# Optimization experiments

Hardware: AMD Instinct MI355X
Metric: run time of the kernel (lower is better)

## Reference

```python
import jax, jax.numpy as jnp
import numpy as np

B, C, T, S, E = 8, 1024, 2048, 2048, 1024
SCALE = 0.7071067811865476  # sqrt(0.5), as in ConvS2S


def setup_inputs() -> dict:
    key = jax.random.key(0)
    ks = jax.random.split(key, 8)
    return {
        "conved": jax.random.normal(ks[0], (B, C, T), jnp.float32),
        "encoder_conved": jax.random.normal(ks[1], (B, S, E), jnp.float32),
        "encoder_combined": jax.random.normal(ks[2], (B, S, E), jnp.float32),
        "x": jax.random.normal(ks[3], (B, T, E), jnp.float32),
        "scale": jnp.float32(SCALE),
        # attn_hid2emb: Linear(out_channels -> emb_dim); torch weight is [out, in]
        "W_h2e": jax.random.normal(ks[4], (E, C), jnp.float32) * 0.02,
        "b_h2e": jnp.zeros((E,), jnp.float32),
        # attn_emb2hid: Linear(emb_dim -> out_channels)
        "W_e2h": jax.random.normal(ks[5], (C, E), jnp.float32) * 0.02,
        "b_e2h": jnp.zeros((C,), jnp.float32),
    }


def reference(conved, encoder_conved, encoder_combined, x, scale,
              W_h2e, b_h2e, W_e2h, b_e2h):
    # conved: [B, C, T] -> project to embedding space: [B, T, E]
    conved_emb = jnp.einsum('bct,ec->bte', conved, W_h2e) + b_h2e
    conved_combined = (conved_emb + x) * scale            # [B, T, E]
    # energy = Q @ K^T : [B, T, S]
    energy = jnp.einsum('bte,bse->bts', conved_combined, encoder_conved)
    attention = jax.nn.softmax(energy, axis=-1)           # [B, T, S]
    # attended encoding = A @ V : [B, T, E]
    attended = jnp.einsum('bts,bse->bte', attention, encoder_combined)
    # project back to hidden: [B, T, C]
    attended = jnp.einsum('bte,ce->btc', attended, W_e2h) + b_e2h
    # residual in channels-first layout: [B, C, T]
    attended_combined = conved + attended.transpose(0, 2, 1)
    return attention, attended_combined
```

## Files before the change

### kernel.cpp

```cpp
#include <hip/hip_runtime.h>
#include <hip/hip_bf16.h>

typedef unsigned short u16;
typedef __attribute__((ext_vector_type(8))) short bf16x8;
typedef __attribute__((ext_vector_type(4))) float f32x4;

#define B_ 8
#define C_ 1024
#define T_ 2048
#define S_ 2048
#define E_ 1024

__device__ __forceinline__ u16 f2bf(float v) {
    __hip_bfloat16 h = __float2bfloat16(v);
    return *reinterpret_cast<u16*>(&h);
}
__device__ __forceinline__ float bf2f(u16 u) {
    __hip_bfloat16 h = *reinterpret_cast<__hip_bfloat16*>(&u);
    return __bfloat162float(h);
}
__device__ __forceinline__ void split2(float v, u16& h, u16& l) {
    h = f2bf(v);
    l = f2bf(v - bf2f(h));
}

__device__ __forceinline__ void async16(const u16* g, u16* l) {
    __builtin_amdgcn_global_load_lds((const __attribute__((address_space(1))) void*)g,
                                     (__attribute__((address_space(3))) void*)l, 16, 0, 0);
}

template<int EPI, bool SPLIT3>
__global__ __launch_bounds__(256, 2) void gemm_bt(
    const u16* __restrict__ Ahi, const u16* __restrict__ Alo,
    const u16* __restrict__ Bhi, const u16* __restrict__ Blo,
    int Kdim, long sA, long sB, int N,
    float* __restrict__ outF, long sOutF,
    u16* __restrict__ outB, u16* __restrict__ outB2, long sOutB,
    const float* __restrict__ bias,
    const float* __restrict__ add, long sAdd,
    const float* __restrict__ scale_ptr)
{
    __shared__ u16 smem[(SPLIT3 ? 4 : 2) * 4096];
    u16* As_hi = smem;
    u16* Bs_hi = smem + 4096;
    u16* As_lo = SPLIT3 ? (smem + 8192)  : smem;
    u16* Bs_lo = SPLIT3 ? (smem + 12288) : smem;

    const int b  = blockIdx.z;
    const int bm = blockIdx.y * 128;
    const int bn = blockIdx.x * 128;
    const u16* Ah = Ahi + (size_t)b * sA;
    const u16* Bh = Bhi + (size_t)b * sB;
    const u16* Al = SPLIT3 ? (Alo + (size_t)b * sA) : nullptr;
    const u16* Bl = SPLIT3 ? (Blo + (size_t)b * sB) : nullptr;

    const int tid  = threadIdx.x;
    const int w    = tid >> 6, lane = tid & 63;
    const int wr   = w >> 1,   wc   = w & 1;
    const int lr   = lane & 15, ls  = lane >> 4;

    const int srow  = lane >> 2;
    const int sslot = lane & 3;
    const int kk    = ((sslot ^ ((srow >> 1) & 3)) << 3);
    const size_t gA0 = (size_t)(bm + w * 16 + srow) * Kdim + kk;
    const size_t gA1 = (size_t)(bm + (w + 4) * 16 + srow) * Kdim + kk;
    const size_t gB0 = (size_t)(bn + w * 16 + srow) * Kdim + kk;
    const size_t gB1 = (size_t)(bn + (w + 4) * 16 + srow) * Kdim + kk;
    const int l0 = w * 512, l1 = (w + 4) * 512;

    f32x4 acc[4][4];
    #pragma unroll
    for (int m = 0; m < 4; m++) {
        #pragma unroll
        for (int n = 0; n < 4; n++) {
            f32x4 z = {0.f, 0.f, 0.f, 0.f};
            acc[m][n] = z;
        }
    }

    const int foff = ((ls ^ ((lr >> 1) & 3)) << 3);

    for (int k0 = 0; k0 < Kdim; k0 += 32) {
        async16(Ah + gA0 + k0, As_hi + l0);
        async16(Ah + gA1 + k0, As_hi + l1);
        async16(Bh + gB0 + k0, Bs_hi + l0);
        async16(Bh + gB1 + k0, Bs_hi + l1);
        if constexpr (SPLIT3) {
            async16(Al + gA0 + k0, As_lo + l0);
            async16(Al + gA1 + k0, As_lo + l1);
            async16(Bl + gB0 + k0, Bs_lo + l0);
            async16(Bl + gB1 + k0, Bs_lo + l1);
        }
        asm volatile("s_waitcnt vmcnt(0)" ::: "memory");
        __syncthreads();

        bf16x8 ah[4], al[4];
        #pragma unroll
        for (int m = 0; m < 4; m++) {
            int off = (wr * 64 + m * 16 + lr) * 32 + foff;
            ah[m] = *(const bf16x8*)(As_hi + off);
            if constexpr (SPLIT3) al[m] = *(const bf16x8*)(As_lo + off);
        }
        #pragma unroll
        for (int n = 0; n < 4; n++) {
            int off = (wc * 64 + n * 16 + lr) * 32 + foff;
            bf16x8 bh = *(const bf16x8*)(Bs_hi + off);
            if constexpr (SPLIT3) {
                bf16x8 bl = *(const bf16x8*)(Bs_lo + off);
                #pragma unroll
                for (int m = 0; m < 4; m++)
                    acc[m][n] = __builtin_amdgcn_mfma_f32_16x16x32_bf16(ah[m], bh, acc[m][n], 0, 0, 0);
                #pragma unroll
                for (int m = 0; m < 4; m++)
                    acc[m][n] = __builtin_amdgcn_mfma_f32_16x16x32_bf16(ah[m], bl, acc[m][n], 0, 0, 0);
                #pragma unroll
                for (int m = 0; m < 4; m++)
                    acc[m][n] = __builtin_amdgcn_mfma_f32_16x16x32_bf16(al[m], bh, acc[m][n], 0, 0, 0);
            } else {
                #pragma unroll
                for (int m = 0; m < 4; m++)
                    acc[m][n] = __builtin_amdgcn_mfma_f32_16x16x32_bf16(ah[m], bh, acc[m][n], 0, 0, 0);
            }
        }
        __syncthreads();
    }

    float scl = 1.0f;
    if constexpr (EPI == 0) scl = *scale_ptr;

    #pragma unroll
    for (int m = 0; m < 4; m++) {
        #pragma unroll
        for (int n = 0; n < 4; n++) {
            const int Rb = bm + wr * 64 + m * 16 + ls * 4;
            const int Cc = bn + wc * 64 + n * 16 + lr;
            f32x4 v = acc[m][n];
            #pragma unroll
            for (int j = 0; j < 4; j++) {
                const int R = Rb + j;
                const size_t o = (size_t)R * N + Cc;
                float val = v[j];
                if constexpr (EPI == 0) {
                    val = (val + bias[Cc] + add[(size_t)b * sAdd + o]) * scl;
                    u16 h, l;
                    split2(val, h, l);
                    outB[(size_t)b * sOutB + o]  = h;
                    outB2[(size_t)b * sOutB + o] = l;
                } else if constexpr (EPI == 1) {
                    outF[(size_t)b * sOutF + o] = val;
                } else if constexpr (EPI == 2) {
                    outB[(size_t)b * sOutB + o] = f2bf(val);
                } else {
                    outF[(size_t)b * sOutF + o] = val + bias[R] + add[(size_t)b * sAdd + o];
                }
            }
        }
    }
}


template<bool SPLIT>
__global__ __launch_bounds__(256) void split_cast_kernel(
    const float* __restrict__ in, u16* __restrict__ hi, u16* __restrict__ lo, long n4)
{
    long i = (long)blockIdx.x * blockDim.x + threadIdx.x;
    long stride = (long)gridDim.x * blockDim.x;
    const float4* in4 = (const float4*)in;
    ushort4* h4 = (ushort4*)hi;
    ushort4* l4 = (ushort4*)lo;
    for (; i < n4; i += stride) {
        float4 v = in4[i];
        ushort4 h, l;
        split2(v.x, h.x, l.x);
        split2(v.y, h.y, l.y);
        split2(v.z, h.z, l.z);
        split2(v.w, h.w, l.w);
        h4[i] = h;
        if constexpr (SPLIT) l4[i] = l;
    }
}

template<bool SPLIT>
__global__ __launch_bounds__(256) void transpose_split_kernel(
    const float* __restrict__ in, u16* __restrict__ hi, u16* __restrict__ lo, int R, int Cc)
{
    __shared__ float tile[32][33];
    const size_t boff = (size_t)blockIdx.z * R * Cc;
    const int c0 = blockIdx.x * 32;
    const int r0 = blockIdx.y * 32;
    const int tx = threadIdx.x, ty = threadIdx.y;
    #pragma unroll
    for (int i = ty; i < 32; i += 8)
        tile[i][tx] = in[boff + (size_t)(r0 + i) * Cc + c0 + tx];
    __syncthreads();
    #pragma unroll
    for (int i = ty; i < 32; i += 8) {
        float v = tile[tx][i];
        size_t o = boff + (size_t)(c0 + i) * R + r0 + tx;
        u16 h, l;
        split2(v, h, l);
        hi[o] = h;
        if constexpr (SPLIT) lo[o] = l;
    }
}

__device__ __forceinline__ float wred_max(float v) {
    #pragma unroll
    for (int off = 32; off; off >>= 1) v = fmaxf(v, __shfl_xor(v, off, 64));
    return v;
}
__device__ __forceinline__ float wred_sum(float v) {
    #pragma unroll
    for (int off = 32; off; off >>= 1) v += __shfl_xor(v, off, 64);
    return v;
}

__global__ __launch_bounds__(256) void softmax_kernel(float* __restrict__ att, u16* __restrict__ attB)
{
    __shared__ float red[4];
    const size_t row = blockIdx.x;
    float* p  = att  + row * (size_t)S_;
    u16*   pb = attB + row * (size_t)S_;
    const int t = threadIdx.x, w = t >> 6, lane = t & 63;

    float4 v0 = ((const float4*)p)[t];
    float4 v1 = ((const float4*)p)[t + 256];
    float m = fmaxf(fmaxf(fmaxf(v0.x, v0.y), fmaxf(v0.z, v0.w)),
                    fmaxf(fmaxf(v1.x, v1.y), fmaxf(v1.z, v1.w)));
    m = wred_max(m);
    if (lane == 0) red[w] = m;
    __syncthreads();
    m = fmaxf(fmaxf(red[0], red[1]), fmaxf(red[2], red[3]));
    __syncthreads();

    float e0 = __expf(v0.x - m), e1 = __expf(v0.y - m), e2 = __expf(v0.z - m), e3 = __expf(v0.w - m);
    float e4 = __expf(v1.x - m), e5 = __expf(v1.y - m), e6 = __expf(v1.z - m), e7 = __expf(v1.w - m);
    float s = ((e0 + e1) + (e2 + e3)) + ((e4 + e5) + (e6 + e7));
    s = wred_sum(s);
    if (lane == 0) red[w] = s;
    __syncthreads();
    s = (red[0] + red[1]) + (red[2] + red[3]);
    const float inv = 1.0f / s;

    float4 o0 = {e0 * inv, e1 * inv, e2 * inv, e3 * inv};
    float4 o1 = {e4 * inv, e5 * inv, e6 * inv, e7 * inv};
    ((float4*)p)[t]       = o0;
    ((float4*)p)[t + 256] = o1;
    ushort4 b0, b1;
    b0.x = f2bf(o0.x); b0.y = f2bf(o0.y); b0.z = f2bf(o0.z); b0.w = f2bf(o0.w);
    b1.x = f2bf(o1.x); b1.y = f2bf(o1.y); b1.z = f2bf(o1.z); b1.w = f2bf(o1.w);
    ((ushort4*)pb)[t]       = b0;
    ((ushort4*)pb)[t + 256] = b1;
}

extern "C" void kernel_launch(void* const* d_in, const int* in_sizes, int n_in,
                              void* d_out, int out_size, void* d_ws, size_t ws_size,
                              hipStream_t stream)
{
    (void)in_sizes; (void)n_in; (void)out_size; (void)ws_size;
    const float* conved = (const float*)d_in[0];
    const float* encK   = (const float*)d_in[1];
    const float* encV   = (const float*)d_in[2];
    const float* x      = (const float*)d_in[3];
    const float* scale  = (const float*)d_in[4];
    const float* W_h2e  = (const float*)d_in[5];
    const float* b_h2e  = (const float*)d_in[6];
    const float* W_e2h  = (const float*)d_in[7];
    const float* b_e2h  = (const float*)d_in[8];

    float* attn = (float*)d_out;
    float* out2 = attn + (size_t)B_ * T_ * S_;

    const size_t NBT = (size_t)B_ * T_ * E_;
    char* p = (char*)d_ws;
    auto take = [&](size_t bytes) { char* r = p; p += bytes; return (u16*)r; };

    u16* Qhi  = take(NBT * 2);
    u16* Qlo  = take(NBT * 2);
    u16* Khi  = take(NBT * 2);
    u16* Klo  = take(NBT * 2);
    u16* Vt   = take(NBT * 2);
    u16* Whi  = take((size_t)E_ * C_ * 2);
    u16* Wlo  = take((size_t)E_ * C_ * 2);
    u16* We2h = take((size_t)C_ * E_ * 2);
    u16* CThi = take(NBT * 2);
    u16* CTlo = take(NBT * 2);
    u16* attnB = CThi;
    u16* Aemb  = Qhi;

    dim3 blk256(256);
    dim3 tblk(32, 8);

    transpose_split_kernel<true ><<<dim3(T_ / 32, C_ / 32, B_), tblk, 0, stream>>>(conved, CThi, CTlo, C_, T_);
    split_cast_kernel<true >     <<<dim3(512),  blk256, 0, stream>>>(W_h2e, Whi, Wlo, (long)E_ * C_ / 4);
    split_cast_kernel<true >     <<<dim3(2048), blk256, 0, stream>>>(encK, Khi, Klo, (long)B_ * S_ * E_ / 4);
    transpose_split_kernel<false><<<dim3(E_ / 32, S_ / 32, B_), tblk, 0, stream>>>(encV, Vt, nullptr, S_, E_);
    split_cast_kernel<false>     <<<dim3(512),  blk256, 0, stream>>>(W_e2h, We2h, nullptr, (long)C_ * E_ / 4);

    gemm_bt<0, true><<<dim3(E_ / 128, T_ / 128, B_), blk256, 0, stream>>>(
        CThi, CTlo, Whi, Wlo, C_, (long)T_ * C_, 0L, E_,
        nullptr, 0L, Qhi, Qlo, (long)T_ * E_, b_h2e, x, (long)T_ * E_, scale);

    gemm_bt<1, true><<<dim3(S_ / 128, T_ / 128, B_), blk256, 0, stream>>>(
        Qhi, Qlo, Khi, Klo, E_, (long)T_ * E_, (long)S_ * E_, S_,
        attn, (long)T_ * S_, nullptr, nullptr, 0L, nullptr, nullptr, 0L, nullptr);

    softmax_kernel<<<dim3(B_ * T_), blk256, 0, stream>>>(attn, attnB);

    gemm_bt<2, false><<<dim3(E_ / 128, T_ / 128, B_), blk256, 0, stream>>>(
        attnB, nullptr, Vt, nullptr, S_, (long)T_ * S_, (long)E_ * S_, E_,
        nullptr, 0L, Aemb, nullptr, (long)T_ * E_, nullptr, nullptr, 0L, nullptr);

    gemm_bt<3, false><<<dim3(T_ / 128, C_ / 128, B_), blk256, 0, stream>>>(
        We2h, nullptr, Aemb, nullptr, E_, 0L, (long)T_ * E_, T_,
        out2, (long)C_ * T_, nullptr, nullptr, 0L, b_e2h, conved, (long)C_ * T_, nullptr);
}
```

Baseline: 935.7 us.

## Remap GEMM tiles across XCDs, raise occupancy hint, vectorize transpose kernel

The GEMM kernel now remaps its flattened block index so that consecutive tiles land on the same XCD, which should improve L2 reuse of A and B rows across the chiplets. Its launch bounds hint also rises from 2 to 4 workgroups per CU, which may force register spilling. The transpose/split kernel switches to float4 loads and ushort4 stores with an 8x32 thread block. The tile reads after the transpose now hit the same LDS bank for lanes with different tx (stride 4*33), which can cause bank conflicts.

```diff
diff --git a/kernel.cpp b/kernel.cpp
--- a/kernel.cpp
+++ b/kernel.cpp
@@ -30,7 +30,7 @@
 }
 
 template<int EPI, bool SPLIT3>
-__global__ __launch_bounds__(256, 2) void gemm_bt(
+__global__ __launch_bounds__(256, 4) void gemm_bt(
     const u16* __restrict__ Ahi, const u16* __restrict__ Alo,
     const u16* __restrict__ Bhi, const u16* __restrict__ Blo,
     int Kdim, long sA, long sB, int N,
@@ -46,9 +46,18 @@
     u16* As_lo = SPLIT3 ? (smem + 8192)  : smem;
     u16* Bs_lo = SPLIT3 ? (smem + 12288) : smem;
 
+    const int gx = gridDim.x;
+    const int nwg = gx * gridDim.y;
+    int f = blockIdx.y * gx + blockIdx.x;
+    {
+        const int q = nwg >> 3, r = nwg & 7;
+        const int xcd = f & 7, idx = f >> 3;
+        f = (xcd < r ? xcd * (q + 1) : r * (q + 1) + (xcd - r) * q) + idx;
+    }
     const int b  = blockIdx.z;
-    const int bm = blockIdx.y * 128;
-    const int bn = blockIdx.x * 128;
+    const int bm = (f / gx) * 128;
+    const int bn = (f % gx) * 128;
+
     const u16* Ah = Ahi + (size_t)b * sA;
     const u16* Bh = Bhi + (size_t)b * sB;
     const u16* Al = SPLIT3 ? (Alo + (size_t)b * sA) : nullptr;
@@ -188,20 +197,24 @@
     const size_t boff = (size_t)blockIdx.z * R * Cc;
     const int c0 = blockIdx.x * 32;
     const int r0 = blockIdx.y * 32;
-    const int tx = threadIdx.x, ty = threadIdx.y;
-    #pragma unroll
-    for (int i = ty; i < 32; i += 8)
-        tile[i][tx] = in[boff + (size_t)(r0 + i) * Cc + c0 + tx];
+    const int tx = threadIdx.x;
+    const int ty = threadIdx.y;
+
+    float4 v = *(const float4*)&in[boff + (size_t)(r0 + ty) * Cc + c0 + 4 * tx];
+    tile[ty][4 * tx + 0] = v.x;
+    tile[ty][4 * tx + 1] = v.y;
+    tile[ty][4 * tx + 2] = v.z;
+    tile[ty][4 * tx + 3] = v.w;
     __syncthreads();
-    #pragma unroll
-    for (int i = ty; i < 32; i += 8) {
-        float v = tile[tx][i];
-        size_t o = boff + (size_t)(c0 + i) * R + r0 + tx;
-        u16 h, l;
-        split2(v, h, l);
-        hi[o] = h;
-        if constexpr (SPLIT) lo[o] = l;
-    }
+
+    ushort4 h, l;
+    split2(tile[4 * tx + 0][ty], h.x, l.x);
+    split2(tile[4 * tx + 1][ty], h.y, l.y);
+    split2(tile[4 * tx + 2][ty], h.z, l.z);
+    split2(tile[4 * tx + 3][ty], h.w, l.w);
+    const size_t o = boff + (size_t)(c0 + ty) * R + r0 + 4 * tx;
+    *(ushort4*)&hi[o] = h;
+    if constexpr (SPLIT) *(ushort4*)&lo[o] = l;
 }
 
 __device__ __forceinline__ float wred_max(float v) {
@@ -289,7 +302,7 @@
     u16* Aemb  = Qhi;
 
     dim3 blk256(256);
-    dim3 tblk(32, 8);
+    dim3 tblk(8, 32);
 
     transpose_split_kernel<true ><<<dim3(T_ / 32, C_ / 32, B_), tblk, 0, stream>>>(conved, CThi, CTlo, C_, T_);
     split_cast_kernel<true >     <<<dim3(512),  blk256, 0, stream>>>(W_h2e, Whi, Wlo, (long)E_ * C_ / 4);
```

After: 917.6 us. No clear change (-1.9%).
